# Optimization experiments

Hardware: AMD Instinct MI355X
Metric: run time of the kernel (lower is better)

## Reference

```python
import jax, jax.numpy as jnp
import numpy as np

B, T, C, H = 2, 2048, 2048, 16
D = C // H  # 128


def _rope(x, cos, sin):
    # x: (B, T, H, D); cos/sin: (T, D//2) -> complex rotation on consecutive pairs
    xr = x.reshape(x.shape[0], x.shape[1], x.shape[2], D // 2, 2)
    x0, x1 = xr[..., 0], xr[..., 1]
    c = cos[None, :, None, :]
    s = sin[None, :, None, :]
    out = jnp.stack([x0 * c - x1 * s, x0 * s + x1 * c], axis=-1)
    return out.reshape(x.shape)


def setup_inputs() -> dict:
    key = jax.random.key(0)
    k1, k2, k3 = jax.random.split(key, 3)
    x = jax.random.normal(k1, (B, T, C), dtype=jnp.float32)
    w_qkv = jax.random.normal(k2, (3 * C, C), dtype=jnp.float32) * (C ** -0.5)
    w_proj = jax.random.normal(k3, (C, C), dtype=jnp.float32) * (C ** -0.5)
    # standard RoPE frequencies: theta_i = 10000^{-2i/D}
    inv_freq = 1.0 / (10000.0 ** (np.arange(0, D, 2, dtype=np.float32) / D))
    ang = np.outer(np.arange(T, dtype=np.float32), inv_freq)  # (T, D//2)
    freqs_cos = jnp.asarray(np.cos(ang), dtype=jnp.float32)
    freqs_sin = jnp.asarray(np.sin(ang), dtype=jnp.float32)
    return {"x": x, "w_qkv": w_qkv, "w_proj": w_proj,
            "freqs_cos": freqs_cos, "freqs_sin": freqs_sin}


def reference(x, w_qkv, w_proj, freqs_cos, freqs_sin):
    b, t, c = x.shape
    qkv = (x @ w_qkv.T).reshape(b, t, 3, H, D)
    q, k, v = qkv[:, :, 0], qkv[:, :, 1], qkv[:, :, 2]  # (B,T,H,D)
    q = _rope(q, freqs_cos, freqs_sin)
    k = _rope(k, freqs_cos, freqs_sin)
    scale = 1.0 / jnp.sqrt(jnp.float32(D))
    scores = jnp.einsum('bqhd,bkhd->bhqk', q, k) * scale  # (B,H,T,T)
    causal = jnp.tril(jnp.ones((t, t), dtype=bool))
    scores = jnp.where(causal[None, None], scores, jnp.finfo(scores.dtype).min)
    attn = jax.nn.softmax(scores, axis=-1)
    out = jnp.einsum('bhqk,bkhd->bqhd', attn, v).reshape(b, t, c)
    return out @ w_proj.T
```

## Files before the change

kernel.cpp:

```cpp
#include <hip/hip_runtime.h>
#include <hip/hip_bf16.h>

typedef float f32x4 __attribute__((ext_vector_type(4)));
typedef __bf16 bf16x8 __attribute__((ext_vector_type(8)));
typedef __bf16 bf16x4 __attribute__((ext_vector_type(4)));

constexpr int B_ = 2, T_ = 2048, C_ = 2048, H_ = 16, D_ = 128;
constexpr int M_ = B_ * T_;
constexpr int NQKV_ = 3 * C_;

__global__ void cvt_kernel(const float* __restrict__ in, __bf16* __restrict__ out, int n4) {
    int i = blockIdx.x * blockDim.x + threadIdx.x;
    int stride = gridDim.x * blockDim.x;
    for (; i < n4; i += stride) {
        float4 v = reinterpret_cast<const float4*>(in)[i];
        bf16x4 o;
        o[0] = (__bf16)v.x; o[1] = (__bf16)v.y; o[2] = (__bf16)v.z; o[3] = (__bf16)v.w;
        reinterpret_cast<bf16x4*>(out)[i] = o;
    }
}

template <typename OutT>
__global__ __launch_bounds__(256, 3) void gemm_bt(
    const __bf16* __restrict__ A, const __bf16* __restrict__ Bm,
    OutT* __restrict__ Cm, int Mdim, int Ndim, int Kdim)
{
    constexpr int BK = 64;
    __shared__ __align__(16) __bf16 As[128 * BK];
    __shared__ __align__(16) __bf16 Bs[128 * BK];
    const int tid = threadIdx.x;
    const int wave = tid >> 6, lane = tid & 63;
    const int fr = lane & 15, fq = lane >> 4;
    const int nbx = Ndim >> 7;
    const int bm = (blockIdx.x / nbx) << 7;
    const int bn = (blockIdx.x % nbx) << 7;
    const int wr = (wave >> 1) * 64, wc = (wave & 1) * 64;
    f32x4 acc[4][4] = {};
    const int srow = tid >> 3;
    const int schunk = tid & 7;

    for (int k0 = 0; k0 < Kdim; k0 += BK) {
        __syncthreads();
        #pragma unroll
        for (int p = 0; p < 4; ++p) {
            int r = p * 32 + srow;
            bf16x8 av = *reinterpret_cast<const bf16x8*>(A + (size_t)(bm + r) * Kdim + k0 + schunk * 8);
            bf16x8 bv = *reinterpret_cast<const bf16x8*>(Bm + (size_t)(bn + r) * Kdim + k0 + schunk * 8);
            int c = (schunk ^ (r & 7)) * 16;
            *reinterpret_cast<bf16x8*>((char*)As + r * 128 + c) = av;
            *reinterpret_cast<bf16x8*>((char*)Bs + r * 128 + c) = bv;
        }
        __syncthreads();
        #pragma unroll
        for (int s = 0; s < 2; ++s) {
            bf16x8 af[4], bg[4];
            #pragma unroll
            for (int m = 0; m < 4; ++m) {
                int row = wr + m * 16 + fr;
                int c = (s * 64 + 16 * fq) ^ ((row & 7) << 4);
                af[m] = *reinterpret_cast<const bf16x8*>((const char*)As + row * 128 + c);
            }
            #pragma unroll
            for (int n = 0; n < 4; ++n) {
                int row = wc + n * 16 + fr;
                int c = (s * 64 + 16 * fq) ^ ((row & 7) << 4);
                bg[n] = *reinterpret_cast<const bf16x8*>((const char*)Bs + row * 128 + c);
            }
            #pragma unroll
            for (int m = 0; m < 4; ++m)
                #pragma unroll
                for (int n = 0; n < 4; ++n)
                    acc[m][n] = __builtin_amdgcn_mfma_f32_16x16x32_bf16(af[m], bg[n], acc[m][n], 0, 0, 0);
        }
    }
    #pragma unroll
    for (int m = 0; m < 4; ++m) {
        #pragma unroll
        for (int n = 0; n < 4; ++n) {
            int row0 = bm + wr + m * 16 + fq * 4;
            int col = bn + wc + n * 16 + fr;
            #pragma unroll
            for (int i = 0; i < 4; ++i)
                Cm[(size_t)(row0 + i) * Ndim + col] = (OutT)acc[m][n][i];
        }
    }
}

__global__ void rope_pack(const __bf16* __restrict__ qkv,
                          const float* __restrict__ fcos, const float* __restrict__ fsin,
                          __bf16* __restrict__ Q, __bf16* __restrict__ K, __bf16* __restrict__ V)
{
    const int row = blockIdx.x;
    const int b = row / T_, t = row % T_;
    for (int idx = threadIdx.x; idx < 3 * C_ / 2; idx += blockDim.x) {
        int s = idx / (C_ / 2);
        int rem = idx % (C_ / 2);
        int h = rem >> 6, j = rem & 63;
        const __bf16* src = qkv + (size_t)row * NQKV_ + (s * H_ + h) * D_ + 2 * j;
        float x0 = (float)src[0], x1 = (float)src[1];
        size_t dst = ((size_t)(b * H_ + h) * T_ + t) * D_ + 2 * j;
        if (s == 2) {
            V[dst] = (__bf16)x0; V[dst + 1] = (__bf16)x1;
        } else {
            float c = fcos[t * 64 + j], sn = fsin[t * 64 + j];
            float o0 = x0 * c - x1 * sn, o1 = x0 * sn + x1 * c;
            if (s == 0) { Q[dst] = (__bf16)o0; Q[dst + 1] = (__bf16)o1; }
            else        { K[dst] = (__bf16)o0; K[dst + 1] = (__bf16)o1; }
        }
    }
}

__global__ void transpose_v(const __bf16* __restrict__ V, __bf16* __restrict__ Vt) {
    const int bid = blockIdx.x;
    const int per_bh = (T_ / 64) * (D_ / 64);
    const int bh = bid / per_bh;
    const int rem = bid % per_bh;
    const int t0 = (rem / (D_ / 64)) * 64;
    const int d0 = (rem % (D_ / 64)) * 64;
    __shared__ __align__(16) __bf16 tile[64][72];
    const int tid = threadIdx.x;
    #pragma unroll
    for (int pass = 0; pass < 2; ++pass) {
        int r = pass * 32 + (tid >> 3);
        int ch = tid & 7;
        *reinterpret_cast<bf16x8*>(&tile[r][ch * 8]) =
            *reinterpret_cast<const bf16x8*>(V + ((size_t)bh * T_ + t0 + r) * D_ + d0 + ch * 8);
    }
    __syncthreads();
    #pragma unroll
    for (int pass = 0; pass < 2; ++pass) {
        int dr = pass * 32 + (tid >> 3);
        int ch = tid & 7;
        bf16x8 v;
        #pragma unroll
        for (int e = 0; e < 8; ++e) v[e] = tile[ch * 8 + e][dr];
        *reinterpret_cast<bf16x8*>(Vt + ((size_t)bh * D_ + d0 + dr) * T_ + t0 + ch * 8) = v;
    }
}

__global__ __launch_bounds__(256, 2) void attn_fwd(
    const __bf16* __restrict__ Q, const __bf16* __restrict__ K,
    const __bf16* __restrict__ Vt, __bf16* __restrict__ Out)
{
    const int bh = blockIdx.x, qt = blockIdx.y;
    const int tid = threadIdx.x;
    const int wave = tid >> 6, lane = tid & 63;
    const int fr = lane & 15, fq = lane >> 4;
    __shared__ __align__(16) __bf16 Ks[64 * 128];
    __shared__ __align__(16) __bf16 Vs[128 * 64];
    __shared__ __align__(16) __bf16 Ps[4][16 * 64];

    bf16x8 qf[4];
    {
        const __bf16* qb = Q + ((size_t)bh * T_ + qt * 64 + wave * 16 + fr) * D_;
        #pragma unroll
        for (int s = 0; s < 4; ++s)
            qf[s] = *reinterpret_cast<const bf16x8*>(qb + s * 32 + 8 * fq);
    }
    f32x4 oacc[8] = {};
    float mrow[4], lrow[4];
    #pragma unroll
    for (int i = 0; i < 4; ++i) { mrow[i] = -3.0e38f; lrow[i] = 0.f; }
    const float scale = 0.08838834764831845f;
    char* pb = (char*)&Ps[wave][0];

    for (int kt = 0; kt <= qt; ++kt) {
        __syncthreads();
        {
            int r = tid >> 4, ch = tid & 15;
            #pragma unroll
            for (int p = 0; p < 4; ++p) {
                int row = p * 16 + r;
                bf16x8 v = *reinterpret_cast<const bf16x8*>(K + ((size_t)bh * T_ + kt * 64 + row) * D_ + ch * 8);
                int c = (ch ^ (row & 7)) * 16;
                *reinterpret_cast<bf16x8*>((char*)Ks + row * 256 + c) = v;
            }
            int r2 = tid >> 3, ch2 = tid & 7;
            #pragma unroll
            for (int p = 0; p < 4; ++p) {
                int row = p * 32 + r2;
                bf16x8 v = *reinterpret_cast<const bf16x8*>(Vt + ((size_t)bh * D_ + row) * T_ + kt * 64 + ch2 * 8);
                int c = (ch2 ^ (row & 7)) * 16;
                *reinterpret_cast<bf16x8*>((char*)Vs + row * 128 + c) = v;
            }
        }
        __syncthreads();

        f32x4 sacc[4] = {};
        #pragma unroll
        for (int s = 0; s < 4; ++s) {
            #pragma unroll
            for (int f = 0; f < 4; ++f) {
                int row = f * 16 + fr;
                int c = (s * 64 + 16 * fq) ^ ((row & 7) << 4);
                bf16x8 kf = *reinterpret_cast<const bf16x8*>((const char*)Ks + row * 256 + c);
                sacc[f] = __builtin_amdgcn_mfma_f32_16x16x32_bf16(qf[s], kf, sacc[f], 0, 0, 0);
            }
        }

        float pm[4];
        #pragma unroll
        for (int i = 0; i < 4; ++i) {
            float mx = -3.0e38f;
            #pragma unroll
            for (int f = 0; f < 4; ++f) {
                float sv = sacc[f][i] * scale;
                if (kt == qt && (f * 16 + fr) > (wave * 16 + fq * 4 + i)) sv = -3.0e38f;
                sacc[f][i] = sv;
                mx = fmaxf(mx, sv);
            }
            pm[i] = mx;
        }
        #pragma unroll
        for (int msk = 1; msk < 16; msk <<= 1)
            #pragma unroll
            for (int i = 0; i < 4; ++i)
                pm[i] = fmaxf(pm[i], __shfl_xor(pm[i], msk, 64));
        float alpha[4], rs[4];
        #pragma unroll
        for (int i = 0; i < 4; ++i) {
            float mn = fmaxf(mrow[i], pm[i]);
            alpha[i] = __expf(mrow[i] - mn);
            mrow[i] = mn;
            rs[i] = 0.f;
        }
        #pragma unroll
        for (int f = 0; f < 4; ++f)
            #pragma unroll
            for (int i = 0; i < 4; ++i) {
                float p = __expf(sacc[f][i] - mrow[i]);
                sacc[f][i] = p;
                rs[i] += p;
            }
        #pragma unroll
        for (int msk = 1; msk < 16; msk <<= 1)
            #pragma unroll
            for (int i = 0; i < 4; ++i)
                rs[i] += __shfl_xor(rs[i], msk, 64);
        #pragma unroll
        for (int i = 0; i < 4; ++i) lrow[i] = lrow[i] * alpha[i] + rs[i];
        #pragma unroll
        for (int n = 0; n < 8; ++n)
            #pragma unroll
            for (int i = 0; i < 4; ++i) oacc[n][i] *= alpha[i];

        #pragma unroll
        for (int f = 0; f < 4; ++f)
            #pragma unroll
            for (int i = 0; i < 4; ++i) {
                int r = fq * 4 + i;
                int bc = ((f * 16 + fr) * 2) ^ ((r & 7) << 4);
                *reinterpret_cast<__bf16*>(pb + r * 128 + bc) = (__bf16)sacc[f][i];
            }
        asm volatile("s_waitcnt lgkmcnt(0)" ::: "memory");

        #pragma unroll
        for (int ks = 0; ks < 2; ++ks) {
            int cp = (ks * 64 + 16 * fq) ^ ((fr & 7) << 4);
            bf16x8 pf = *reinterpret_cast<const bf16x8*>(pb + fr * 128 + cp);
            #pragma unroll
            for (int n = 0; n < 8; ++n) {
                int d = n * 16 + fr;
                int cv = (ks * 64 + 16 * fq) ^ ((d & 7) << 4);
                bf16x8 vf = *reinterpret_cast<const bf16x8*>((const char*)Vs + d * 128 + cv);
                oacc[n] = __builtin_amdgcn_mfma_f32_16x16x32_bf16(pf, vf, oacc[n], 0, 0, 0);
            }
        }
    }

    const int b = bh >> 4, h = bh & 15;
    #pragma unroll
    for (int n = 0; n < 8; ++n) {
        int d = n * 16 + fr;
        #pragma unroll
        for (int i = 0; i < 4; ++i) {
            int tg = qt * 64 + wave * 16 + fq * 4 + i;
            Out[((size_t)b * T_ + tg) * C_ + h * D_ + d] = (__bf16)(oacc[n][i] / lrow[i]);
        }
    }
}

extern "C" void kernel_launch(void* const* d_in, const int* in_sizes, int n_in,
                              void* d_out, int out_size, void* d_ws, size_t ws_size,
                              hipStream_t stream) {
    const float* x = (const float*)d_in[0];
    const float* w_qkv = (const float*)d_in[1];
    const float* w_proj = (const float*)d_in[2];
    const float* fcos = (const float*)d_in[3];
    const float* fsin = (const float*)d_in[4];
    float* out = (float*)d_out;

    char* ws = (char*)d_ws;
    size_t o = 0;
    __bf16* xb     = (__bf16*)(ws + o); o += (size_t)M_ * C_ * 2;
    __bf16* wqkvb  = (__bf16*)(ws + o); o += (size_t)NQKV_ * C_ * 2;
    __bf16* wprojb = (__bf16*)(ws + o); o += (size_t)C_ * C_ * 2;
    __bf16* qkvb   = (__bf16*)(ws + o); o += (size_t)M_ * NQKV_ * 2;
    __bf16* Qb     = (__bf16*)(ws + o); o += (size_t)M_ * C_ * 2;
    __bf16* Kb     = (__bf16*)(ws + o); o += (size_t)M_ * C_ * 2;
    __bf16* Vb     = wqkvb;
    __bf16* Vtb    = xb;
    __bf16* attnb  = qkvb;

    cvt_kernel<<<2048, 256, 0, stream>>>(x, xb, M_ * C_ / 4);
    cvt_kernel<<<2048, 256, 0, stream>>>(w_qkv, wqkvb, NQKV_ * C_ / 4);
    cvt_kernel<<<2048, 256, 0, stream>>>(w_proj, wprojb, C_ * C_ / 4);
    gemm_bt<__bf16><<<(M_ / 128) * (NQKV_ / 128), 256, 0, stream>>>(xb, wqkvb, qkvb, M_, NQKV_, C_);
    rope_pack<<<M_, 256, 0, stream>>>(qkvb, fcos, fsin, Qb, Kb, Vb);
    transpose_v<<<B_ * H_ * (T_ / 64) * (D_ / 64), 256, 0, stream>>>(Vb, Vtb);
    attn_fwd<<<dim3(B_ * H_, T_ / 64), 256, 0, stream>>>(Qb, Kb, Vtb, attnb);
    gemm_bt<float><<<(M_ / 128) * (C_ / 128), 256, 0, stream>>>(attnb, wprojb, out, M_, C_, C_);
}
```

Before: 447.1 us.

## Use direct global-to-LDS loads, vectorize RoPE, and enlarge attention query tiles

GEMM and attention tile loads now use global_load_lds, which writes straight into shared memory without passing through registers. The GEMM drops its XOR swizzle, so LDS reads may hit bank conflicts. Attention now processes 128 query rows per block with 32 rows per wave, computes S transposed, launches the heaviest causal tiles first, and raises wave priority around the MFMA sections. RoPE packing uses one 16-byte vector per thread instead of scalar pairs. Together these aim to cut register staging, K/V reloads and scalar memory traffic, at the cost of more registers and fully masked waves idling on diagonal tiles.

```diff
diff --git a/kernel.cpp b/kernel.cpp
--- a/kernel.cpp
+++ b/kernel.cpp
@@ -8,6 +8,13 @@
 constexpr int B_ = 2, T_ = 2048, C_ = 2048, H_ = 16, D_ = 128;
 constexpr int M_ = B_ * T_;
 constexpr int NQKV_ = 3 * C_;
+
+__device__ __forceinline__ void gload_lds16(const void* g, void* l) {
+    __builtin_amdgcn_global_load_lds(
+        (const __attribute__((address_space(1))) unsigned int*)g,
+        (__attribute__((address_space(3))) unsigned int*)l,
+        16, 0, 0);
+}
 
 __global__ void cvt_kernel(const float* __restrict__ in, __bf16* __restrict__ out, int n4) {
     int i = blockIdx.x * blockDim.x + threadIdx.x;
@@ -25,9 +32,8 @@
     const __bf16* __restrict__ A, const __bf16* __restrict__ Bm,
     OutT* __restrict__ Cm, int Mdim, int Ndim, int Kdim)
 {
-    constexpr int BK = 64;
-    __shared__ __align__(16) __bf16 As[128 * BK];
-    __shared__ __align__(16) __bf16 Bs[128 * BK];
+    __shared__ __align__(16) __bf16 As[128 * 64];
+    __shared__ __align__(16) __bf16 Bs[128 * 64];
     const int tid = threadIdx.x;
     const int wave = tid >> 6, lane = tid & 63;
     const int fr = lane & 15, fq = lane >> 4;
@@ -36,36 +42,28 @@
     const int bn = (blockIdx.x % nbx) << 7;
     const int wr = (wave >> 1) * 64, wc = (wave & 1) * 64;
     f32x4 acc[4][4] = {};
-    const int srow = tid >> 3;
-    const int schunk = tid & 7;
-
-    for (int k0 = 0; k0 < Kdim; k0 += BK) {
+    const int srow = (wave << 5) + (lane >> 3);
+    const int sch = lane & 7;
+    const __bf16* Ag = A + (size_t)(bm + srow) * Kdim + sch * 8;
+    const __bf16* Bg = Bm + (size_t)(bn + srow) * Kdim + sch * 8;
+
+    for (int k0 = 0; k0 < Kdim; k0 += 64) {
         __syncthreads();
         #pragma unroll
         for (int p = 0; p < 4; ++p) {
-            int r = p * 32 + srow;
-            bf16x8 av = *reinterpret_cast<const bf16x8*>(A + (size_t)(bm + r) * Kdim + k0 + schunk * 8);
-            bf16x8 bv = *reinterpret_cast<const bf16x8*>(Bm + (size_t)(bn + r) * Kdim + k0 + schunk * 8);
-            int c = (schunk ^ (r & 7)) * 16;
-            *reinterpret_cast<bf16x8*>((char*)As + r * 128 + c) = av;
-            *reinterpret_cast<bf16x8*>((char*)Bs + r * 128 + c) = bv;
+            gload_lds16(Ag + (size_t)(8 * p) * Kdim + k0, (char*)As + (wave * 32 + 8 * p) * 128);
+            gload_lds16(Bg + (size_t)(8 * p) * Kdim + k0, (char*)Bs + (wave * 32 + 8 * p) * 128);
         }
         __syncthreads();
         #pragma unroll
         for (int s = 0; s < 2; ++s) {
             bf16x8 af[4], bg[4];
             #pragma unroll
-            for (int m = 0; m < 4; ++m) {
-                int row = wr + m * 16 + fr;
-                int c = (s * 64 + 16 * fq) ^ ((row & 7) << 4);
-                af[m] = *reinterpret_cast<const bf16x8*>((const char*)As + row * 128 + c);
-            }
-            #pragma unroll
-            for (int n = 0; n < 4; ++n) {
-                int row = wc + n * 16 + fr;
-                int c = (s * 64 + 16 * fq) ^ ((row & 7) << 4);
-                bg[n] = *reinterpret_cast<const bf16x8*>((const char*)Bs + row * 128 + c);
-            }
+            for (int m = 0; m < 4; ++m)
+                af[m] = *reinterpret_cast<const bf16x8*>((const char*)As + (wr + m * 16 + fr) * 128 + s * 64 + fq * 16);
+            #pragma unroll
+            for (int n = 0; n < 4; ++n)
+                bg[n] = *reinterpret_cast<const bf16x8*>((const char*)Bs + (wc + n * 16 + fr) * 128 + s * 64 + fq * 16);
             #pragma unroll
             for (int m = 0; m < 4; ++m)
                 #pragma unroll
@@ -91,22 +89,32 @@
                           __bf16* __restrict__ Q, __bf16* __restrict__ K, __bf16* __restrict__ V)
 {
     const int row = blockIdx.x;
-    const int b = row / T_, t = row % T_;
-    for (int idx = threadIdx.x; idx < 3 * C_ / 2; idx += blockDim.x) {
-        int s = idx / (C_ / 2);
-        int rem = idx % (C_ / 2);
-        int h = rem >> 6, j = rem & 63;
-        const __bf16* src = qkv + (size_t)row * NQKV_ + (s * H_ + h) * D_ + 2 * j;
-        float x0 = (float)src[0], x1 = (float)src[1];
-        size_t dst = ((size_t)(b * H_ + h) * T_ + t) * D_ + 2 * j;
+    const int b = row >> 11, t = row & (T_ - 1);
+    const int tid = threadIdx.x;
+    const int h = tid >> 4;
+    const int jq = tid & 15;
+    const float4 c4 = *reinterpret_cast<const float4*>(fcos + t * 64 + jq * 4);
+    const float4 s4 = *reinterpret_cast<const float4*>(fsin + t * 64 + jq * 4);
+    const float cc[4] = {c4.x, c4.y, c4.z, c4.w};
+    const float ss[4] = {s4.x, s4.y, s4.z, s4.w};
+    const __bf16* src = qkv + (size_t)row * NQKV_ + h * D_ + jq * 8;
+    const size_t doff = ((size_t)(b * H_ + h) * T_ + t) * D_ + jq * 8;
+    #pragma unroll
+    for (int s = 0; s < 3; ++s) {
+        bf16x8 v = *reinterpret_cast<const bf16x8*>(src + s * C_);
+        bf16x8 o;
         if (s == 2) {
-            V[dst] = (__bf16)x0; V[dst + 1] = (__bf16)x1;
+            o = v;
         } else {
-            float c = fcos[t * 64 + j], sn = fsin[t * 64 + j];
-            float o0 = x0 * c - x1 * sn, o1 = x0 * sn + x1 * c;
-            if (s == 0) { Q[dst] = (__bf16)o0; Q[dst + 1] = (__bf16)o1; }
-            else        { K[dst] = (__bf16)o0; K[dst + 1] = (__bf16)o1; }
-        }
+            #pragma unroll
+            for (int e = 0; e < 4; ++e) {
+                float x0 = (float)v[2 * e], x1 = (float)v[2 * e + 1];
+                o[2 * e]     = (__bf16)(x0 * cc[e] - x1 * ss[e]);
+                o[2 * e + 1] = (__bf16)(x0 * ss[e] + x1 * cc[e]);
+            }
+        }
+        __bf16* dst = (s == 0) ? Q : ((s == 1) ? K : V);
+        *reinterpret_cast<bf16x8*>(dst + doff) = o;
     }
 }
 
@@ -142,140 +150,144 @@
     const __bf16* __restrict__ Q, const __bf16* __restrict__ K,
     const __bf16* __restrict__ Vt, __bf16* __restrict__ Out)
 {
-    const int bh = blockIdx.x, qt = blockIdx.y;
+    const int bh = blockIdx.x;
+    const int qt = (T_ / 128 - 1) - blockIdx.y;
     const int tid = threadIdx.x;
     const int wave = tid >> 6, lane = tid & 63;
     const int fr = lane & 15, fq = lane >> 4;
     __shared__ __align__(16) __bf16 Ks[64 * 128];
     __shared__ __align__(16) __bf16 Vs[128 * 64];
-    __shared__ __align__(16) __bf16 Ps[4][16 * 64];
-
-    bf16x8 qf[4];
-    {
-        const __bf16* qb = Q + ((size_t)bh * T_ + qt * 64 + wave * 16 + fr) * D_;
-        #pragma unroll
-        for (int s = 0; s < 4; ++s)
-            qf[s] = *reinterpret_cast<const bf16x8*>(qb + s * 32 + 8 * fq);
-    }
-    f32x4 oacc[8] = {};
-    float mrow[4], lrow[4];
-    #pragma unroll
-    for (int i = 0; i < 4; ++i) { mrow[i] = -3.0e38f; lrow[i] = 0.f; }
+    __shared__ __align__(16) __bf16 Ps[4][32 * 64];
+
+    const int q0 = qt * 128 + wave * 32;
+    bf16x8 qf[2][4];
+    #pragma unroll
+    for (int m = 0; m < 2; ++m)
+        #pragma unroll
+        for (int ks = 0; ks < 4; ++ks)
+            qf[m][ks] = *reinterpret_cast<const bf16x8*>(
+                Q + ((size_t)bh * T_ + q0 + m * 16 + fr) * D_ + ks * 32 + 8 * fq);
+
+    f32x4 oacc[2][8] = {};
+    float mrow[2] = {-3.0e38f, -3.0e38f}, lrow[2] = {0.f, 0.f};
     const float scale = 0.08838834764831845f;
     char* pb = (char*)&Ps[wave][0];
-
-    for (int kt = 0; kt <= qt; ++kt) {
+    const int qmax = q0 + 31;
+    const int ktmax = 2 * qt + 1;
+    const int kr = lane >> 4, kch = lane & 15;
+    const int vr = lane >> 3, vch = lane & 7;
+
+    for (int kt = 0; kt <= ktmax; ++kt) {
         __syncthreads();
-        {
-            int r = tid >> 4, ch = tid & 15;
-            #pragma unroll
-            for (int p = 0; p < 4; ++p) {
-                int row = p * 16 + r;
-                bf16x8 v = *reinterpret_cast<const bf16x8*>(K + ((size_t)bh * T_ + kt * 64 + row) * D_ + ch * 8);
-                int c = (ch ^ (row & 7)) * 16;
-                *reinterpret_cast<bf16x8*>((char*)Ks + row * 256 + c) = v;
-            }
-            int r2 = tid >> 3, ch2 = tid & 7;
-            #pragma unroll
-            for (int p = 0; p < 4; ++p) {
-                int row = p * 32 + r2;
-                bf16x8 v = *reinterpret_cast<const bf16x8*>(Vt + ((size_t)bh * D_ + row) * T_ + kt * 64 + ch2 * 8);
-                int c = (ch2 ^ (row & 7)) * 16;
-                *reinterpret_cast<bf16x8*>((char*)Vs + row * 128 + c) = v;
-            }
+        #pragma unroll
+        for (int p = 0; p < 4; ++p) {
+            int row = 16 * wave + 4 * p + kr;
+            gload_lds16(K + ((size_t)bh * T_ + kt * 64 + row) * D_ + ((kch ^ (row & 7)) << 3),
+                        (char*)Ks + (16 * wave + 4 * p) * 256);
+        }
+        #pragma unroll
+        for (int p = 0; p < 4; ++p) {
+            int row = 32 * wave + 8 * p + vr;
+            gload_lds16(Vt + ((size_t)bh * D_ + row) * T_ + kt * 64 + ((vch ^ (row & 7)) << 3),
+                        (char*)Vs + (32 * wave + 8 * p) * 128);
         }
         __syncthreads();
-
-        f32x4 sacc[4] = {};
-        #pragma unroll
-        for (int s = 0; s < 4; ++s) {
+        if (kt * 64 > qmax) continue;
+
+        f32x4 sacc[2][4] = {};
+        __builtin_amdgcn_s_setprio(1);
+        #pragma unroll
+        for (int ks = 0; ks < 4; ++ks) {
             #pragma unroll
             for (int f = 0; f < 4; ++f) {
                 int row = f * 16 + fr;
-                int c = (s * 64 + 16 * fq) ^ ((row & 7) << 4);
-                bf16x8 kf = *reinterpret_cast<const bf16x8*>((const char*)Ks + row * 256 + c);
-                sacc[f] = __builtin_amdgcn_mfma_f32_16x16x32_bf16(qf[s], kf, sacc[f], 0, 0, 0);
-            }
-        }
-
-        float pm[4];
-        #pragma unroll
-        for (int i = 0; i < 4; ++i) {
+                bf16x8 kf = *reinterpret_cast<const bf16x8*>(
+                    (const char*)Ks + row * 256 + (((ks * 4 + fq) ^ (fr & 7)) << 4));
+                sacc[0][f] = __builtin_amdgcn_mfma_f32_16x16x32_bf16(kf, qf[0][ks], sacc[0][f], 0, 0, 0);
+                sacc[1][f] = __builtin_amdgcn_mfma_f32_16x16x32_bf16(kf, qf[1][ks], sacc[1][f], 0, 0, 0);
+            }
+        }
+        __builtin_amdgcn_s_setprio(0);
+
+        const bool diag = (kt >= 2 * qt);
+        #pragma unroll
+        for (int m = 0; m < 2; ++m) {
+            const int qg = q0 + m * 16 + fr;
+            const int r = m * 16 + fr;
             float mx = -3.0e38f;
             #pragma unroll
+            for (int f = 0; f < 4; ++f)
+                #pragma unroll
+                for (int i = 0; i < 4; ++i) {
+                    float sv = sacc[m][f][i] * scale;
+                    if (diag && (kt * 64 + f * 16 + fq * 4 + i) > qg) sv = -3.0e38f;
+                    sacc[m][f][i] = sv;
+                    mx = fmaxf(mx, sv);
+                }
+            mx = fmaxf(mx, __shfl_xor(mx, 16, 64));
+            mx = fmaxf(mx, __shfl_xor(mx, 32, 64));
+            float mn = fmaxf(mrow[m], mx);
+            float al = __expf(mrow[m] - mn);
+            mrow[m] = mn;
+            float rs = 0.f;
+            #pragma unroll
             for (int f = 0; f < 4; ++f) {
-                float sv = sacc[f][i] * scale;
-                if (kt == qt && (f * 16 + fr) > (wave * 16 + fq * 4 + i)) sv = -3.0e38f;
-                sacc[f][i] = sv;
-                mx = fmaxf(mx, sv);
-            }
-            pm[i] = mx;
-        }
-        #pragma unroll
-        for (int msk = 1; msk < 16; msk <<= 1)
-            #pragma unroll
-            for (int i = 0; i < 4; ++i)
-                pm[i] = fmaxf(pm[i], __shfl_xor(pm[i], msk, 64));
-        float alpha[4], rs[4];
-        #pragma unroll
-        for (int i = 0; i < 4; ++i) {
-            float mn = fmaxf(mrow[i], pm[i]);
-            alpha[i] = __expf(mrow[i] - mn);
-            mrow[i] = mn;
-            rs[i] = 0.f;
-        }
-        #pragma unroll
-        for (int f = 0; f < 4; ++f)
-            #pragma unroll
-            for (int i = 0; i < 4; ++i) {
-                float p = __expf(sacc[f][i] - mrow[i]);
-                sacc[f][i] = p;
-                rs[i] += p;
-            }
-        #pragma unroll
-        for (int msk = 1; msk < 16; msk <<= 1)
-            #pragma unroll
-            for (int i = 0; i < 4; ++i)
-                rs[i] += __shfl_xor(rs[i], msk, 64);
-        #pragma unroll
-        for (int i = 0; i < 4; ++i) lrow[i] = lrow[i] * alpha[i] + rs[i];
-        #pragma unroll
-        for (int n = 0; n < 8; ++n)
-            #pragma unroll
-            for (int i = 0; i < 4; ++i) oacc[n][i] *= alpha[i];
-
-        #pragma unroll
-        for (int f = 0; f < 4; ++f)
-            #pragma unroll
-            for (int i = 0; i < 4; ++i) {
-                int r = fq * 4 + i;
-                int bc = ((f * 16 + fr) * 2) ^ ((r & 7) << 4);
-                *reinterpret_cast<__bf16*>(pb + r * 128 + bc) = (__bf16)sacc[f][i];
-            }
-        asm volatile("s_waitcnt lgkmcnt(0)" ::: "memory");
-
+                bf16x4 pv;
+                #pragma unroll
+                for (int i = 0; i < 4; ++i) {
+                    float p = __expf(sacc[m][f][i] - mn);
+                    rs += p;
+                    pv[i] = (__bf16)p;
+                }
+                *reinterpret_cast<bf16x4*>(pb + r * 128 + ((f * 32 + fq * 8) ^ ((fr & 7) << 4))) = pv;
+            }
+            rs += __shfl_xor(rs, 16, 64);
+            rs += __shfl_xor(rs, 32, 64);
+            lrow[m] = lrow[m] * al + rs;
+            float av[4];
+            #pragma unroll
+            for (int i = 0; i < 4; ++i) av[i] = __shfl(al, fq * 4 + i, 16);
+            #pragma unroll
+            for (int n = 0; n < 8; ++n)
+                #pragma unroll
+                for (int i = 0; i < 4; ++i) oacc[m][n][i] *= av[i];
+        }
+
+        __builtin_amdgcn_s_setprio(1);
         #pragma unroll
         for (int ks = 0; ks < 2; ++ks) {
-            int cp = (ks * 64 + 16 * fq) ^ ((fr & 7) << 4);
-            bf16x8 pf = *reinterpret_cast<const bf16x8*>(pb + fr * 128 + cp);
+            bf16x8 pa[2];
+            #pragma unroll
+            for (int m = 0; m < 2; ++m) {
+                int r = m * 16 + fr;
+                pa[m] = *reinterpret_cast<const bf16x8*>(pb + r * 128 + ((ks * 64 + fq * 16) ^ ((fr & 7) << 4)));
+            }
             #pragma unroll
             for (int n = 0; n < 8; ++n) {
                 int d = n * 16 + fr;
-                int cv = (ks * 64 + 16 * fq) ^ ((d & 7) << 4);
-                bf16x8 vf = *reinterpret_cast<const bf16x8*>((const char*)Vs + d * 128 + cv);
-                oacc[n] = __builtin_amdgcn_mfma_f32_16x16x32_bf16(pf, vf, oacc[n], 0, 0, 0);
-            }
-        }
+                bf16x8 vf = *reinterpret_cast<const bf16x8*>(
+                    (const char*)Vs + d * 128 + (((ks * 4 + fq) ^ (fr & 7)) << 4));
+                oacc[0][n] = __builtin_amdgcn_mfma_f32_16x16x32_bf16(pa[0], vf, oacc[0][n], 0, 0, 0);
+                oacc[1][n] = __builtin_amdgcn_mfma_f32_16x16x32_bf16(pa[1], vf, oacc[1][n], 0, 0, 0);
+            }
+        }
+        __builtin_amdgcn_s_setprio(0);
     }
 
     const int b = bh >> 4, h = bh & 15;
     #pragma unroll
-    for (int n = 0; n < 8; ++n) {
-        int d = n * 16 + fr;
-        #pragma unroll
-        for (int i = 0; i < 4; ++i) {
-            int tg = qt * 64 + wave * 16 + fq * 4 + i;
-            Out[((size_t)b * T_ + tg) * C_ + h * D_ + d] = (__bf16)(oacc[n][i] / lrow[i]);
+    for (int m = 0; m < 2; ++m) {
+        float linv[4];
+        #pragma unroll
+        for (int i = 0; i < 4; ++i) linv[i] = 1.0f / __shfl(lrow[m], fq * 4 + i, 16);
+        #pragma unroll
+        for (int n = 0; n < 8; ++n) {
+            int d = n * 16 + fr;
+            #pragma unroll
+            for (int i = 0; i < 4; ++i) {
+                int tg = qt * 128 + wave * 32 + m * 16 + fq * 4 + i;
+                Out[((size_t)b * T_ + tg) * C_ + h * D_ + d] = (__bf16)(oacc[m][n][i] * linv[i]);
+            }
         }
     }
 }
@@ -308,6 +320,6 @@
     gemm_bt<__bf16><<<(M_ / 128) * (NQKV_ / 128), 256, 0, stream>>>(xb, wqkvb, qkvb, M_, NQKV_, C_);
     rope_pack<<<M_, 256, 0, stream>>>(qkvb, fcos, fsin, Qb, Kb, Vb);
     transpose_v<<<B_ * H_ * (T_ / 64) * (D_ / 64), 256, 0, stream>>>(Vb, Vtb);
-    attn_fwd<<<dim3(B_ * H_, T_ / 64), 256, 0, stream>>>(Qb, Kb, Vtb, attnb);
+    attn_fwd<<<dim3(B_ * H_, T_ / 128), 256, 0, stream>>>(Qb, Kb, Vtb, attnb);
     gemm_bt<float><<<(M_ / 128) * (C_ / 128), 256, 0, stream>>>(attnb, wprojb, out, M_, C_, C_);
 }
```

Measured after the change: 409.3 us. -8.5%, faster.
